# Kernel optimization log

Measured on AMD Instinct MI355X. Metric: run time of the kernel, lower is better.

Reference implementation:

```python
import jax, jax.numpy as jnp
import numpy as np

NUM_GRAPHS = 1024
NODES = 1024          # nodes per graph (ring length)
N = NUM_GRAPHS * NODES
H = 64


def setup_inputs() -> dict:
    key = jax.random.key(0)
    ks = jax.random.split(key, 4)
    node_index = jax.random.normal(ks[0], (N, 3), dtype=jnp.float32)
    # per-graph ring edges (intended behavior of the torch code)
    i = jnp.arange(N, dtype=jnp.int64)
    g = i // NODES
    src = i
    dst = g * NODES + (i + 1) % NODES
    edge_index = jnp.stack([src, dst])  # [2, N]
    # glorot-ish weights, zero biases (PyG GCNConv default bias=True)
    W1 = jax.random.normal(ks[1], (3, H), dtype=jnp.float32) * (1.0 / np.sqrt(3.0))
    b1 = jnp.zeros((H,), dtype=jnp.float32)
    W2 = jax.random.normal(ks[2], (H, H), dtype=jnp.float32) * (1.0 / np.sqrt(H))
    b2 = jnp.zeros((H,), dtype=jnp.float32)
    Wl = jax.random.normal(ks[3], (H, 3), dtype=jnp.float32) * (1.0 / np.sqrt(H))
    bl = jnp.zeros((3,), dtype=jnp.float32)
    return {"node_index": node_index, "edge_index": edge_index,
            "W1": W1, "b1": b1, "W2": W2, "b2": b2, "Wl": Wl, "bl": bl}


def gcn_layer(x, W, b, src, dst):
    """PyG GCNConv: symmetric-normalized aggregation with self-loops.
    out[j] = sum_{i->j} (deg_i * deg_j)^-0.5 * (x_i @ W) + b
    """
    n = x.shape[0]
    h = x @ W                                   # [n, out]
    loop = jnp.arange(n, dtype=src.dtype)
    s = jnp.concatenate([src, loop])
    d = jnp.concatenate([dst, loop])
    deg = jax.ops.segment_sum(jnp.ones(d.shape[0], dtype=h.dtype), d, num_segments=n)
    dinv = jnp.where(deg > 0, jax.lax.rsqrt(jnp.maximum(deg, 1e-12)), 0.0)
    norm = dinv[s] * dinv[d]                    # [E+n]
    msg = h[s] * norm[:, None]                  # gather + scale
    out = jax.ops.segment_sum(msg, d, num_segments=n)  # scatter-add
    return out + b


def reference(node_index, edge_index, W1, b1, W2, b2, Wl, bl):
    src, dst = edge_index[0], edge_index[1]
    x = jax.nn.relu(gcn_layer(node_index, W1, b1, src, dst))
    x = jax.nn.relu(gcn_layer(x, W2, b2, src, dst))
    return x @ Wl + bl
```

## Files before the change

### kernel.cpp

```cpp
#include <hip/hip_runtime.h>

#define NPG 1024
#define NT 256
#define PITCH 88

typedef _Float16 half8 __attribute__((ext_vector_type(8)));
typedef _Float16 half4v __attribute__((ext_vector_type(4)));
typedef __fp16 fp16x2 __attribute__((ext_vector_type(2)));
typedef float floatx4 __attribute__((ext_vector_type(4)));
typedef unsigned int uint4v __attribute__((ext_vector_type(4)));

#define WS_W2F 0
#define WS_W1F 4096
#define WS_WLF 5120

__device__ __forceinline__ unsigned short f2h(float f) {
    union { _Float16 h; unsigned short u; } v; v.h = (_Float16)f; return v.u;
}
__device__ __forceinline__ float h2f(unsigned short u) {
    union { unsigned short u; _Float16 h; } v; v.u = u; return (float)v.h;
}
__device__ __forceinline__ unsigned int pack_h2(float a, float b) {
    union { fp16x2 h; unsigned int u; } v;
    v.h = __builtin_amdgcn_cvt_pkrtz(a, b);
    return v.u;
}
__device__ __forceinline__ int kperm(int k) {
    return ((k & 3)) | (((k >> 2) & 3) << 4) | (((k >> 4) & 3) << 2);
}

union Frag  { half8 h;  unsigned int u[4]; };
union Frag4 { half4v h; unsigned int u[2]; };

__global__ void gnn_prep(const float* __restrict__ W1,
                         const float* __restrict__ b1,
                         const float* __restrict__ W2,
                         const float* __restrict__ Wl,
                         unsigned short* __restrict__ ws)
{
    int idx = blockIdx.x * NT + threadIdx.x;
    if (idx >= 6144) return;
    float v;
    if (idx < 4096) {
        int l = (idx >> 3) & 63, j = idx & 7;
        int c16l = l & 15, quadl = l >> 4;
        int f = idx >> 9, ct = f >> 1, kb = f & 1;
        int o  = ct * 16 + c16l;
        int k  = kperm(kb * 32 + quadl * 8 + j);
        v = 0.5f * W2[k * 64 + o];
    } else if (idx < 5120) {
        int r = idx - 4096;
        int ct = r >> 8, rem = r & 255;
        int l = rem >> 2, j = rem & 3;
        int c16l = l & 15, quadl = l >> 4;
        v = 0.0f;
        if (quadl == 0)
            v = (j < 3) ? W1[j * 64 + ct * 16 + c16l] : b1[ct * 16 + c16l];
    } else {
        int r = idx - 5120;
        int l = (r >> 3) & 63, j = r & 7;
        int c16l = l & 15, quadl = l >> 4;
        int kb = r >> 9;
        int o = (2 * kb + (j >> 2)) * 16 + quadl * 4 + (j & 3);
        v = (c16l < 3) ? Wl[o * 3 + c16l] : 0.0f;
    }
    ws[idx] = f2h(v);
}

__global__ __launch_bounds__(NT, 4)
void gnn_main(const float* __restrict__ x0,
              const float* __restrict__ b2,
              const float* __restrict__ bl,
              const unsigned short* __restrict__ ws,
              float* __restrict__ out)
{
    __shared__ unsigned short X1w[4][16 * PITCH];
    __shared__ uint2 ySv[513];

    const int t    = threadIdx.x;
    const int lane = t & 63;
    const int w    = t >> 6;
    const int c16  = lane & 15;
    const int quad = lane >> 4;

    const int g     = blockIdx.x >> 1;
    const int base  = (blockIdx.x & 1) * 512;
    const int gbase = g * NPG;

    #pragma unroll
    for (int rr = 0; rr < 2; rr++) {
        int rl = t + rr * 256;
        int n1 = (base - 1 + rl) & (NPG - 1);
        int n0 = (n1 - 1) & (NPG - 1);
        const float* a = x0 + (gbase + n0) * 3;
        const float* b = x0 + (gbase + n1) * 3;
        uint2 pv;
        pv.x = pack_h2(0.5f * (a[0] + b[0]), 0.5f * (a[1] + b[1]));
        pv.y = pack_h2(0.5f * (a[2] + b[2]), 1.0f);
        ySv[rl] = pv;
    }
    if (t == 0) {
        int n1 = (base + 511) & (NPG - 1);
        int n0 = (n1 - 1) & (NPG - 1);
        const float* a = x0 + (gbase + n0) * 3;
        const float* b = x0 + (gbase + n1) * 3;
        uint2 pv;
        pv.x = pack_h2(0.5f * (a[0] + b[0]), 0.5f * (a[1] + b[1]));
        pv.y = pack_h2(0.5f * (a[2] + b[2]), 1.0f);
        ySv[512] = pv;
    }

    Frag4 w1f[4];
    #pragma unroll
    for (int ct = 0; ct < 4; ct++)
        w1f[ct].h = *(const half4v*)(ws + WS_W1F + ct * 256 + lane * 4);
    Frag a2[4][2];
    #pragma unroll
    for (int ct = 0; ct < 4; ct++)
        #pragma unroll
        for (int kb = 0; kb < 2; kb++)
            a2[ct][kb].h = *(const half8*)(ws + WS_W2F + (ct * 2 + kb) * 512 + lane * 8);
    Frag a3[2];
    #pragma unroll
    for (int kb = 0; kb < 2; kb++)
        a3[kb].h = *(const half8*)(ws + WS_WLF + kb * 512 + lane * 8);
    floatx4 b2v[4];
    #pragma unroll
    for (int ct = 0; ct < 4; ct++)
        b2v[ct] = *(const floatx4*)(b2 + ct * 16 + quad * 4);
    const float blv = (c16 < 3) ? bl[c16] : 0.0f;

    __syncthreads();

    unsigned short* Xp = &X1w[w][0];
    const int rowoff = c16 * PITCH;

    #pragma unroll 1
    for (int i = 0; i < 8; i++) {
        const int r = i * 64 + 16 * w + c16;

        Frag4 ba, bb;
        ba.u[0] = ba.u[1] = bb.u[0] = bb.u[1] = 0;
        if (quad == 0) {
            uint2 pva = ySv[r];     ba.u[0] = pva.x; ba.u[1] = pva.y;
            uint2 pvb = ySv[r + 1]; bb.u[0] = pvb.x; bb.u[1] = pvb.y;
        }
        unsigned int sw[8];
        #pragma unroll
        for (int ct = 0; ct < 4; ct++) {
            floatx4 z = {0.0f, 0.0f, 0.0f, 0.0f};
            floatx4 aa = __builtin_amdgcn_mfma_f32_16x16x16f16(w1f[ct].h, ba.h, z, 0, 0, 0);
            floatx4 ab = __builtin_amdgcn_mfma_f32_16x16x16f16(w1f[ct].h, bb.h, z, 0, 0, 0);
            Frag4 va, vb;
            va.u[0] = pack_h2(aa[0], aa[1]); va.u[1] = pack_h2(aa[2], aa[3]);
            vb.u[0] = pack_h2(ab[0], ab[1]); vb.u[1] = pack_h2(ab[2], ab[3]);
            half4v z4 = {};
            va.h = __builtin_elementwise_max(va.h, z4);
            vb.h = __builtin_elementwise_max(vb.h, z4);
            va.h = va.h + vb.h;
            sw[2 * ct]     = va.u[0];
            sw[2 * ct + 1] = va.u[1];
        }
        uint4v v0, v1;
        v0.x = sw[0]; v0.y = sw[1]; v0.z = sw[2]; v0.w = sw[3];
        v1.x = sw[4]; v1.y = sw[5]; v1.z = sw[6]; v1.w = sw[7];
        *(uint4v*)&Xp[rowoff + 16 * quad]     = v0;
        *(uint4v*)&Xp[rowoff + 16 * quad + 8] = v1;

        half8 bsum0 = *(const half8*)&Xp[rowoff + quad * 8];
        half8 bsum1 = *(const half8*)&Xp[rowoff + 32 + quad * 8];

        floatx4 acc2[4];
        #pragma unroll
        for (int ct = 0; ct < 4; ct++) {
            floatx4 z = b2v[ct];
            z = __builtin_amdgcn_mfma_f32_16x16x32_f16(a2[ct][0].h, bsum0, z, 0, 0, 0);
            z = __builtin_amdgcn_mfma_f32_16x16x32_f16(a2[ct][1].h, bsum1, z, 0, 0, 0);
            acc2[ct] = z;
        }
        Frag pa[2];
        #pragma unroll
        for (int ct = 0; ct < 4; ct++) {
            pa[ct >> 1].u[(ct & 1) * 2    ] = pack_h2(acc2[ct][0], acc2[ct][1]);
            pa[ct >> 1].u[(ct & 1) * 2 + 1] = pack_h2(acc2[ct][2], acc2[ct][3]);
        }
        half8 z8 = {};
        pa[0].h = __builtin_elementwise_max(pa[0].h, z8);
        pa[1].h = __builtin_elementwise_max(pa[1].h, z8);
        floatx4 acc3 = {0.0f, 0.0f, 0.0f, 0.0f};
        acc3 = __builtin_amdgcn_mfma_f32_16x16x32_f16(pa[0].h, a3[0].h, acc3, 0, 0, 0);
        acc3 = __builtin_amdgcn_mfma_f32_16x16x32_f16(pa[1].h, a3[1].h, acc3, 0, 0, 0);
        if (c16 < 3) {
            float* po = out + (gbase + base + i * 64 + 16 * w + quad * 4) * 3 + c16;
            po[0] = acc3[0] + blv;
            po[3] = acc3[1] + blv;
            po[6] = acc3[2] + blv;
            po[9] = acc3[3] + blv;
        }
    }
}

extern "C" void kernel_launch(void* const* d_in, const int* in_sizes, int n_in,
                              void* d_out, int out_size, void* d_ws, size_t ws_size,
                              hipStream_t stream) {
    const float* x0 = (const float*)d_in[0];
    const float* W1 = (const float*)d_in[2];
    const float* b1 = (const float*)d_in[3];
    const float* W2 = (const float*)d_in[4];
    const float* b2 = (const float*)d_in[5];
    const float* Wl = (const float*)d_in[6];
    const float* bl = (const float*)d_in[7];
    unsigned short* ws = (unsigned short*)d_ws;
    float* out = (float*)d_out;

    gnn_prep<<<24, NT, 0, stream>>>(W1, b1, W2, Wl, ws);
    gnn_main<<<2048, NT, 0, stream>>>(x0, b2, bl, ws, out);
}
```

Measured before the change: 98.24 us.

## Reuse layer-1 MFMA results across rows via DPP shift instead of recomputing neighbors

Each wave now owns a contiguous 128-row strip and walks it backwards, so it computes one layer-1 MFMA per 16-row tile instead of two (self and neighbor). The neighbor contribution comes from shifting the previous tile's packed results one lane with a DPP row move, carrying the boundary row from the prior tile. The LDS pitch is also reduced. This halves the layer-1 MFMA and conversion work but adds a serial dependency between tiles and cross-lane data movement that must be correct at tile boundaries.

```diff
diff --git a/kernel.cpp b/kernel.cpp
--- a/kernel.cpp
+++ b/kernel.cpp
@@ -2,10 +2,11 @@
 
 #define NPG 1024
 #define NT 256
-#define PITCH 88
+#define PITCH 72
 
 typedef _Float16 half8 __attribute__((ext_vector_type(8)));
 typedef _Float16 half4v __attribute__((ext_vector_type(4)));
+typedef _Float16 half2v __attribute__((ext_vector_type(2)));
 typedef __fp16 fp16x2 __attribute__((ext_vector_type(2)));
 typedef float floatx4 __attribute__((ext_vector_type(4)));
 typedef unsigned int uint4v __attribute__((ext_vector_type(4)));
@@ -16,14 +17,22 @@
 
 __device__ __forceinline__ unsigned short f2h(float f) {
     union { _Float16 h; unsigned short u; } v; v.h = (_Float16)f; return v.u;
-}
-__device__ __forceinline__ float h2f(unsigned short u) {
-    union { unsigned short u; _Float16 h; } v; v.u = u; return (float)v.h;
 }
 __device__ __forceinline__ unsigned int pack_h2(float a, float b) {
     union { fp16x2 h; unsigned int u; } v;
     v.h = __builtin_amdgcn_cvt_pkrtz(a, b);
     return v.u;
+}
+__device__ __forceinline__ unsigned int pmax0(unsigned int a) {
+    union { half2v h; unsigned int u; } x; x.u = a;
+    half2v z = {};
+    x.h = __builtin_elementwise_max(x.h, z);
+    return x.u;
+}
+__device__ __forceinline__ unsigned int padd(unsigned int a, unsigned int b) {
+    union { half2v h; unsigned int u; } x, y; x.u = a; y.u = b;
+    x.h = x.h + y.h;
+    return x.u;
 }
 __device__ __forceinline__ int kperm(int k) {
     return ((k & 3)) | (((k >> 2) & 3) << 4) | (((k >> 4) & 3) << 2);
@@ -134,64 +143,70 @@
 
     unsigned short* Xp = &X1w[w][0];
     const int rowoff = c16 * PITCH;
-
-    #pragma unroll 1
-    for (int i = 0; i < 8; i++) {
-        const int r = i * 64 + 16 * w + c16;
-
-        Frag4 ba, bb;
-        ba.u[0] = ba.u[1] = bb.u[0] = bb.u[1] = 0;
+    const int wbase  = 128 * w;
+
+    auto l1pack = [&](int row0, unsigned int* p) {
+        Frag4 bfr;
+        bfr.u[0] = bfr.u[1] = 0;
         if (quad == 0) {
-            uint2 pva = ySv[r];     ba.u[0] = pva.x; ba.u[1] = pva.y;
-            uint2 pvb = ySv[r + 1]; bb.u[0] = pvb.x; bb.u[1] = pvb.y;
-        }
-        unsigned int sw[8];
+            int idx = row0 + c16;
+            idx = idx > 512 ? 512 : idx;
+            uint2 pv = ySv[idx];
+            bfr.u[0] = pv.x; bfr.u[1] = pv.y;
+        }
         #pragma unroll
         for (int ct = 0; ct < 4; ct++) {
             floatx4 z = {0.0f, 0.0f, 0.0f, 0.0f};
-            floatx4 aa = __builtin_amdgcn_mfma_f32_16x16x16f16(w1f[ct].h, ba.h, z, 0, 0, 0);
-            floatx4 ab = __builtin_amdgcn_mfma_f32_16x16x16f16(w1f[ct].h, bb.h, z, 0, 0, 0);
-            Frag4 va, vb;
-            va.u[0] = pack_h2(aa[0], aa[1]); va.u[1] = pack_h2(aa[2], aa[3]);
-            vb.u[0] = pack_h2(ab[0], ab[1]); vb.u[1] = pack_h2(ab[2], ab[3]);
-            half4v z4 = {};
-            va.h = __builtin_elementwise_max(va.h, z4);
-            vb.h = __builtin_elementwise_max(vb.h, z4);
-            va.h = va.h + vb.h;
-            sw[2 * ct]     = va.u[0];
-            sw[2 * ct + 1] = va.u[1];
+            floatx4 a = __builtin_amdgcn_mfma_f32_16x16x16f16(w1f[ct].h, bfr.h, z, 0, 0, 0);
+            p[2 * ct]     = pmax0(pack_h2(a[0], a[1]));
+            p[2 * ct + 1] = pmax0(pack_h2(a[2], a[3]));
+        }
+    };
+
+    unsigned int p_prev[8], p_cur[8];
+    l1pack(wbase + 128, p_prev);
+    l1pack(wbase + 112, p_cur);
+
+    #pragma unroll 1
+    for (int i = 7; i >= 0; --i) {
+        const int r0 = wbase + 16 * i;
+
+        unsigned int bs[8];
+        #pragma unroll
+        for (int r = 0; r < 8; r++) {
+            unsigned int s = (c16 == 0) ? p_prev[r] : p_cur[r];
+            unsigned int sh = (unsigned int)__builtin_amdgcn_mov_dpp((int)s, 0x12F, 0xf, 0xf, true);
+            bs[r] = padd(p_cur[r], sh);
+            p_prev[r] = p_cur[r];
         }
         uint4v v0, v1;
-        v0.x = sw[0]; v0.y = sw[1]; v0.z = sw[2]; v0.w = sw[3];
-        v1.x = sw[4]; v1.y = sw[5]; v1.z = sw[6]; v1.w = sw[7];
+        v0.x = bs[0]; v0.y = bs[1]; v0.z = bs[2]; v0.w = bs[3];
+        v1.x = bs[4]; v1.y = bs[5]; v1.z = bs[6]; v1.w = bs[7];
         *(uint4v*)&Xp[rowoff + 16 * quad]     = v0;
         *(uint4v*)&Xp[rowoff + 16 * quad + 8] = v1;
 
+        if (i) l1pack(r0 - 16, p_cur);
+
         half8 bsum0 = *(const half8*)&Xp[rowoff + quad * 8];
         half8 bsum1 = *(const half8*)&Xp[rowoff + 32 + quad * 8];
 
         floatx4 acc2[4];
         #pragma unroll
         for (int ct = 0; ct < 4; ct++) {
-            floatx4 z = b2v[ct];
-            z = __builtin_amdgcn_mfma_f32_16x16x32_f16(a2[ct][0].h, bsum0, z, 0, 0, 0);
-            z = __builtin_amdgcn_mfma_f32_16x16x32_f16(a2[ct][1].h, bsum1, z, 0, 0, 0);
-            acc2[ct] = z;
+            floatx4 z = __builtin_amdgcn_mfma_f32_16x16x32_f16(a2[ct][0].h, bsum0, b2v[ct], 0, 0, 0);
+            acc2[ct]  = __builtin_amdgcn_mfma_f32_16x16x32_f16(a2[ct][1].h, bsum1, z, 0, 0, 0);
         }
         Frag pa[2];
         #pragma unroll
         for (int ct = 0; ct < 4; ct++) {
-            pa[ct >> 1].u[(ct & 1) * 2    ] = pack_h2(acc2[ct][0], acc2[ct][1]);
-            pa[ct >> 1].u[(ct & 1) * 2 + 1] = pack_h2(acc2[ct][2], acc2[ct][3]);
-        }
-        half8 z8 = {};
-        pa[0].h = __builtin_elementwise_max(pa[0].h, z8);
-        pa[1].h = __builtin_elementwise_max(pa[1].h, z8);
+            pa[ct >> 1].u[(ct & 1) * 2    ] = pmax0(pack_h2(acc2[ct][0], acc2[ct][1]));
+            pa[ct >> 1].u[(ct & 1) * 2 + 1] = pmax0(pack_h2(acc2[ct][2], acc2[ct][3]));
+        }
         floatx4 acc3 = {0.0f, 0.0f, 0.0f, 0.0f};
         acc3 = __builtin_amdgcn_mfma_f32_16x16x32_f16(pa[0].h, a3[0].h, acc3, 0, 0, 0);
         acc3 = __builtin_amdgcn_mfma_f32_16x16x32_f16(pa[1].h, a3[1].h, acc3, 0, 0, 0);
         if (c16 < 3) {
-            float* po = out + (gbase + base + i * 64 + 16 * w + quad * 4) * 3 + c16;
+            float* po = out + (gbase + base + r0 + quad * 4) * 3 + c16;
             po[0] = acc3[0] + blv;
             po[3] = acc3[1] + blv;
             po[6] = acc3[2] + blv;
```

Result: no change. 97.77 us (-0.5%).
